# Optimization experiments

Hardware: AMD Instinct MI355X
Metric: run time of the kernel (lower is better)

Reference implementation:

```python
import jax, jax.numpy as jnp
import numpy as np

MODEL_DIM = 1024
TOTAL_DIM = 1024
N_HEADS = 16
HEAD_DIM = TOTAL_DIM // N_HEADS


def setup_inputs() -> dict:
    key = jax.random.key(0)
    k1, k2, k3 = jax.random.split(key, 3)
    query = jax.random.normal(k1, (2, 2048, MODEL_DIM), dtype=jnp.float32)
    # nn.Linear(model_dim, 3*total_dim, bias=False): store as [in, out] for x @ W
    W_in = jax.random.normal(k2, (MODEL_DIM, 3 * TOTAL_DIM), dtype=jnp.float32) / np.sqrt(MODEL_DIM)
    W_out = jax.random.normal(k3, (TOTAL_DIM, MODEL_DIM), dtype=jnp.float32) / np.sqrt(TOTAL_DIM)
    return {"query": query, "W_in": W_in, "W_out": W_out}


def reference(query, W_in, W_out):
    B, S, _ = query.shape
    qkv = query @ W_in                      # [B, S, 3*D]
    q, k, v = jnp.split(qkv, 3, axis=-1)    # each [B, S, D]

    def to_heads(t):
        return t.reshape(B, S, N_HEADS, HEAD_DIM).transpose(0, 2, 1, 3)  # [B,H,S,d]

    q, k, v = to_heads(q), to_heads(k), to_heads(v)
    scale = 1.0 / np.sqrt(HEAD_DIM).astype(np.float32)
    scores = jnp.einsum('bhqd,bhkd->bhqk', q, k) * scale  # [B,H,S,S]
    causal = jnp.tril(jnp.ones((S, S), dtype=bool))
    scores = jnp.where(causal, scores, jnp.finfo(scores.dtype).min)
    probs = jax.nn.softmax(scores, axis=-1)
    attn = jnp.einsum('bhqk,bhkd->bhqd', probs, v)        # [B,H,S,d]
    attn = attn.transpose(0, 2, 1, 3).reshape(B, S, TOTAL_DIM)
    return attn @ W_out                     # [B, S, model_dim]
```

## Files before the change

kernel.cpp:

```cpp
#include <hip/hip_runtime.h>


typedef __bf16 bf16x8 __attribute__((ext_vector_type(8)));
typedef __bf16 bf16x4 __attribute__((ext_vector_type(4)));
typedef short s16x4 __attribute__((ext_vector_type(4)));
typedef float f32x4 __attribute__((ext_vector_type(4)));
typedef int i32x2 __attribute__((ext_vector_type(2)));

#define B_   2
#define S_   2048
#define DM   1024
#define NH   16
#define HD   64
#define N3   3072
#define M_   4096

#define SCALE_LOG2E 0.180336884f

__device__ __forceinline__ unsigned short f2bf(float f) {
  unsigned int u = __float_as_uint(f);
  u += 0x7fffu + ((u >> 16) & 1u);
  return (unsigned short)(u >> 16);
}

__device__ __forceinline__ void gload_lds16(void* lds, const void* g) {
  __builtin_amdgcn_global_load_lds(
      (__attribute__((address_space(1))) void*)g,
      (__attribute__((address_space(3))) void*)lds, 16, 0, 0);
}

__device__ __forceinline__ f32x4 mfma16(bf16x4 a, bf16x4 b, f32x4 c) {
#if __has_builtin(__builtin_amdgcn_mfma_f32_16x16x16_bf16)
  return __builtin_amdgcn_mfma_f32_16x16x16_bf16(a, b, c, 0, 0, 0);
#else
  return __builtin_amdgcn_mfma_f32_16x16x16bf16_1k(
      __builtin_bit_cast(s16x4, a), __builtin_bit_cast(s16x4, b), c, 0, 0, 0);
#endif
}

__global__ __launch_bounds__(256) void f32_to_bf16_vec(
    const float4* __restrict__ in, unsigned short* __restrict__ out, int n4) {
  int i = blockIdx.x * 256 + threadIdx.x;
  if (i < n4) {
    float4 v = in[i];
    ushort4 o;
    o.x = f2bf(v.x); o.y = f2bf(v.y); o.z = f2bf(v.z); o.w = f2bf(v.w);
    *(ushort4*)(&out[(size_t)i * 4]) = o;
  }
}

__global__ __launch_bounds__(256) void transpose_f32_bf16(
    const float* __restrict__ in, unsigned short* __restrict__ out, int R, int C,
    int scale_rows, float scale) {
  __shared__ float tile[32][33];
  const int tx = threadIdx.x, ty = threadIdx.y;
  const int x = blockIdx.x * 32 + tx;
  const int y0 = blockIdx.y * 32;
#pragma unroll
  for (int j = 0; j < 32; j += 8)
    tile[ty + j][tx] = in[(size_t)(y0 + ty + j) * C + x];
  __syncthreads();
  const int ox = y0 + tx;
  const int oy0 = blockIdx.x * 32;
#pragma unroll
  for (int j = 0; j < 32; j += 8) {
    const int orow = oy0 + ty + j;
    float v = tile[tx][ty + j];
    if (orow < scale_rows) v *= scale;
    out[(size_t)orow * R + ox] = f2bf(v);
  }
}

__global__ __launch_bounds__(256) void transpose_v(
    const unsigned short* __restrict__ qkv, unsigned short* __restrict__ vTn) {
  __shared__ unsigned short tile[64][72];
  const int kt = blockIdx.x;
  const int h  = blockIdx.y;
  const int b  = blockIdx.z;
  const int t  = threadIdx.x;
  const int row = t >> 3;
  const int c8  = (t & 7) * 8;
#pragma unroll
  for (int rr = 0; rr < 2; rr++) {
    const int s = row + rr * 32;
    const size_t src = (size_t)(b * S_ + kt * 64 + s) * N3 + 2 * DM + h * HD + c8;
    *(float4*)&tile[s][c8] = *(const float4*)&qkv[src];
  }
  __syncthreads();
  const size_t base = (size_t)((b * NH + h) * 32 + kt) * 4096;
#pragma unroll
  for (int u0 = 0; u0 < 2; u0++) {
    const int u = t + u0 * 256;
    const int p = u >> 8, d = (u >> 2) & 63, q = u & 3;
    const int s0 = 32 * p + q * 4;
    ushort4 w0, w1;
    w0.x = tile[s0 + 0][d];  w0.y = tile[s0 + 1][d];
    w0.z = tile[s0 + 2][d];  w0.w = tile[s0 + 3][d];
    w1.x = tile[s0 + 16][d]; w1.y = tile[s0 + 17][d];
    w1.z = tile[s0 + 18][d]; w1.w = tile[s0 + 19][d];
    *(ushort4*)&vTn[base + (size_t)u * 8]     = w0;
    *(ushort4*)&vTn[base + (size_t)u * 8 + 4] = w1;
  }
}

template <int OUT_BF16>
__global__ __launch_bounds__(256) void gemm_abt(
    const unsigned short* __restrict__ A, const unsigned short* __restrict__ Bt,
    void* __restrict__ Cv, int M, int N, int K) {
  __shared__ __align__(16) unsigned short a_sm[128 * 32];
  __shared__ __align__(16) unsigned short b_sm[128 * 32];
  const int tid = threadIdx.x;
  const int lane = tid & 63, wave = tid >> 6;
  const int quad = lane >> 4, l15 = lane & 15;
  const int row0 = blockIdx.y * 128, col0 = blockIdx.x * 128;
  const int wm = (wave >> 1) * 64, wn = (wave & 1) * 64;

  f32x4 acc[4][4];
#pragma unroll
  for (int i = 0; i < 4; i++)
#pragma unroll
    for (int j = 0; j < 4; j++) acc[i][j] = (f32x4){0.f, 0.f, 0.f, 0.f};

  const int e0 = tid * 8;

  for (int k0 = 0; k0 < K; k0 += 32) {
    __syncthreads();
#pragma unroll
    for (int i = 0; i < 2; i++) {
      int e = e0 + i * 2048;
      int r = e >> 5, c = e & 31;
      gload_lds16(&a_sm[e], &A[(size_t)(row0 + r) * K + k0 + c]);
      gload_lds16(&b_sm[e], &Bt[(size_t)(col0 + r) * K + k0 + c]);
    }
    __syncthreads();

    bf16x8 af[4], bfb[4];
#pragma unroll
    for (int i = 0; i < 4; i++) {
      af[i]  = *(const bf16x8*)&a_sm[(wm + i * 16 + l15) * 32 + quad * 8];
      bfb[i] = *(const bf16x8*)&b_sm[(wn + i * 16 + l15) * 32 + quad * 8];
    }
#pragma unroll
    for (int i = 0; i < 4; i++)
#pragma unroll
      for (int j = 0; j < 4; j++)
        acc[i][j] = __builtin_amdgcn_mfma_f32_16x16x32_bf16(af[i], bfb[j], acc[i][j], 0, 0, 0);
  }

#pragma unroll
  for (int i = 0; i < 4; i++) {
#pragma unroll
    for (int j = 0; j < 4; j++) {
#pragma unroll
      for (int r = 0; r < 4; r++) {
        const int row = row0 + wm + i * 16 + quad * 4 + r;
        const int col = col0 + wn + j * 16 + l15;
        const float v = acc[i][j][r];
        if (OUT_BF16)
          ((unsigned short*)Cv)[(size_t)row * N + col] = f2bf(v);
        else
          ((float*)Cv)[(size_t)row * N + col] = v;
      }
    }
  }
}

__global__ __launch_bounds__(512, 4) void attn_fused11(
    const unsigned short* __restrict__ qkv,
    const unsigned short* __restrict__ vTn,
    unsigned short* __restrict__ attnout) {
  const int h = blockIdx.y, b = blockIdx.z;
  const int j = blockIdx.x;
  const int tid = threadIdx.x;
  const int lane = tid & 63, wave = tid >> 6;
  const int quad = lane >> 4, l15 = lane & 15;
  const int sw = l15 & 7;

  __shared__ __align__(16) unsigned short k_sm[4 * 4096];
  __shared__ __align__(16) unsigned short vt_sm[4 * 4096];

  const int wrow0 = (wave < 4) ? (j * 64 + wave * 16)
                               : ((31 - j) * 64 + (wave - 4) * 16);
  const int qrow = wrow0 + l15;

  bf16x8 qf[2];
  {
    const unsigned short* qp = qkv + (size_t)(b * S_ + qrow) * N3 + h * HD + quad * 8;
    qf[0] = *(const bf16x8*)qp;
    qf[1] = *(const bf16x8*)(qp + 32);
  }

  f32x4 o[4];
#pragma unroll
  for (int n = 0; n < 4; n++) o[n] = (f32x4){0.f, 0.f, 0.f, 0.f};
  float lsum = 0.f;

  const int r0s = tid >> 3;
  const int gch = ((tid & 7) ^ (r0s & 7)) * 8;
  const unsigned short* kgb = qkv + (size_t)(b * S_ + r0s) * N3 + DM + h * HD + gch;
  const unsigned short* vgl = vTn + (size_t)((b * NH + h) * 32) * 4096 + tid * 8;

  const int nt = 32 - j;

  int pk[4][2];
  const unsigned short* vbp = &vt_sm[0];

  auto PV = [&]() {
#pragma unroll
    for (int p = 0; p < 2; p++) {
      i32x2 wlo, whi;
      wlo.x = pk[2 * p][0];     wlo.y = pk[2 * p][1];
      whi.x = pk[2 * p + 1][0]; whi.y = pk[2 * p + 1][1];
      const bf16x4 blo = __builtin_bit_cast(bf16x4, wlo);
      const bf16x4 bhi = __builtin_bit_cast(bf16x4, whi);
#pragma unroll
      for (int mb = 0; mb < 4; mb++) {
        const bf16x8 vv =
            *(const bf16x8*)&vbp[(p * 256 + mb * 64 + l15 * 4 + quad) * 8];
        bf16x4 alo, ahi;
#pragma unroll
        for (int i = 0; i < 4; i++) { alo[i] = vv[i]; ahi[i] = vv[i + 4]; }
        o[mb] = mfma16(alo, blo, o[mb]);
        o[mb] = mfma16(ahi, bhi, o[mb]);
      }
    }
  };

  gload_lds16(&k_sm[tid * 8], kgb);
  gload_lds16(&vt_sm[tid * 8], vgl);
  gload_lds16(&k_sm[4096 + tid * 8], kgb + (size_t)64 * N3);
  gload_lds16(&vt_sm[4096 + tid * 8], vgl + 4096);

  for (int t = 0; t < nt; t++) {
    if (t + 1 < nt) asm volatile("s_waitcnt vmcnt(2)" ::: "memory");
    else            asm volatile("s_waitcnt vmcnt(0)" ::: "memory");
    __builtin_amdgcn_s_barrier();
    __builtin_amdgcn_sched_barrier(0);
    if (t + 2 < nt) {
      const int b2 = (t + 2) & 3;
      gload_lds16(&k_sm[b2 * 4096 + tid * 8], kgb + (size_t)(t + 2) * 64 * N3);
      gload_lds16(&vt_sm[b2 * 4096 + tid * 8], vgl + (size_t)(t + 2) * 4096);
    }
    const unsigned short* kb = &k_sm[(t & 3) * 4096];
    const unsigned short* vb = &vt_sm[(t & 3) * 4096];

    if (t >= 1 && (t - 1) * 64 <= wrow0 + 15) PV();

    if (t * 64 <= wrow0 + 15) {
      f32x4 s[4];
#pragma unroll
      for (int mb = 0; mb < 4; mb++) s[mb] = (f32x4){0.f, 0.f, 0.f, 0.f};
#pragma unroll
      for (int mb = 0; mb < 4; mb++) {
        const int ro = (mb * 16 + l15) * 64;
        bf16x8 kf0 = *(const bf16x8*)&kb[ro + ((quad ^ sw) << 3)];
        bf16x8 kf1 = *(const bf16x8*)&kb[ro + (((4 + quad) ^ sw) << 3)];
        s[mb] = __builtin_amdgcn_mfma_f32_16x16x32_bf16(kf0, qf[0], s[mb], 0, 0, 0);
        s[mb] = __builtin_amdgcn_mfma_f32_16x16x32_bf16(kf1, qf[1], s[mb], 0, 0, 0);
      }

      if (t * 64 + 63 <= wrow0) {
#pragma unroll
        for (int mb = 0; mb < 4; mb++)
#pragma unroll
          for (int r = 0; r < 4; r++)
            s[mb][r] = exp2f(s[mb][r]);
      } else {
        const int kq0 = t * 64 + quad * 4;
#pragma unroll
        for (int mb = 0; mb < 4; mb++)
#pragma unroll
          for (int r = 0; r < 4; r++) {
            const float e = exp2f(s[mb][r]);
            s[mb][r] = (kq0 + mb * 16 + r <= qrow) ? e : 0.f;
          }
      }
#pragma unroll
      for (int mb = 0; mb < 4; mb++)
        lsum += (s[mb][0] + s[mb][1]) + (s[mb][2] + s[mb][3]);

#pragma unroll
      for (int mb = 0; mb < 4; mb++) {
        const unsigned u0 = __float_as_uint(s[mb][0]) + 0x8000u;
        const unsigned u1 = __float_as_uint(s[mb][1]) + 0x8000u;
        const unsigned u2 = __float_as_uint(s[mb][2]) + 0x8000u;
        const unsigned u3 = __float_as_uint(s[mb][3]) + 0x8000u;
        pk[mb][0] = (int)__builtin_amdgcn_perm(u1, u0, 0x07060302u);
        pk[mb][1] = (int)__builtin_amdgcn_perm(u3, u2, 0x07060302u);
      }
      vbp = vb;
    }
  }

  if ((nt - 1) * 64 <= wrow0 + 15) PV();

  asm volatile("s_waitcnt vmcnt(0)" ::: "memory");

  float l = lsum;
  l += __shfl_xor(l, 16);
  l += __shfl_xor(l, 32);
  const float inv = 1.0f / l;
  const size_t grow = (size_t)(b * S_ + qrow);
#pragma unroll
  for (int mb = 0; mb < 4; mb++) {
    ushort4 w;
    w.x = f2bf(o[mb][0] * inv);
    w.y = f2bf(o[mb][1] * inv);
    w.z = f2bf(o[mb][2] * inv);
    w.w = f2bf(o[mb][3] * inv);
    *(ushort4*)&attnout[grow * DM + h * HD + mb * 16 + quad * 4] = w;
  }
}

extern "C" void kernel_launch(void* const* d_in, const int* in_sizes, int n_in,
                              void* d_out, int out_size, void* d_ws, size_t ws_size,
                              hipStream_t stream) {
  const float* query = (const float*)d_in[0];
  const float* w_in  = (const float*)d_in[1];
  const float* w_out = (const float*)d_in[2];
  float* out = (float*)d_out;

  char* ws = (char*)d_ws;
  unsigned short* qbf     = (unsigned short*)(ws);
  unsigned short* vTn     = (unsigned short*)(ws);
  unsigned short* w_in_t  = (unsigned short*)(ws + 8388608);
  unsigned short* w_out_t = (unsigned short*)(ws + 14680064);
  unsigned short* qkv     = (unsigned short*)(ws + 16777216);
  unsigned short* attn    = (unsigned short*)(ws + 41943040);

  f32_to_bf16_vec<<<dim3(M_ * DM / 1024), dim3(256), 0, stream>>>(
      (const float4*)query, qbf, M_ * DM / 4);
  transpose_f32_bf16<<<dim3(N3 / 32, DM / 32), dim3(32, 8), 0, stream>>>(
      w_in, w_in_t, DM, N3, DM, SCALE_LOG2E);
  transpose_f32_bf16<<<dim3(DM / 32, DM / 32), dim3(32, 8), 0, stream>>>(
      w_out, w_out_t, DM, DM, 0, 1.0f);
  gemm_abt<1><<<dim3(N3 / 128, M_ / 128), dim3(256), 0, stream>>>(qbf, w_in_t, qkv, M_, N3, DM);
  transpose_v<<<dim3(32, NH, B_), dim3(256), 0, stream>>>(qkv, vTn);
  attn_fused11<<<dim3(16, NH, B_), dim3(512), 0, stream>>>(qkv, vTn, attn);
  gemm_abt<0><<<dim3(DM / 128, M_ / 128), dim3(256), 0, stream>>>(attn, w_out_t, out, M_, DM, DM);
}
```

Before: 198.8 us.

## Use 64-row tiles for output GEMM, add MFMA priority and hardware bf16 pack

Replaces the output projection GEMM with a 64x128-tile variant, doubling the grid to 512 blocks so more CUs are busy on the 4096x1024 problem. In attention, the MFMA sections are wrapped with s_setprio so waves issuing matrix ops get scheduling priority. The manual add-and-permute bf16 packing is replaced with the v_cvt_pk_bf16_f32 instruction, which uses round-to-nearest-even instead of round-half-up. The new GEMM has no double buffering and synchronises twice per K step, which may cost latency hiding.

```diff
diff --git a/kernel.cpp b/kernel.cpp
--- a/kernel.cpp
+++ b/kernel.cpp
@@ -36,6 +36,12 @@
   return __builtin_amdgcn_mfma_f32_16x16x16bf16_1k(
       __builtin_bit_cast(s16x4, a), __builtin_bit_cast(s16x4, b), c, 0, 0, 0);
 #endif
+}
+
+__device__ __forceinline__ int cvtpk(float s0, float s1) {
+  int r;
+  asm("v_cvt_pk_bf16_f32 %0, %1, %2" : "=v"(r) : "v"(s0), "v"(s1));
+  return r;
 }
 
 __global__ __launch_bounds__(256) void f32_to_bf16_vec(
@@ -165,7 +171,68 @@
   }
 }
 
-__global__ __launch_bounds__(512, 4) void attn_fused11(
+__global__ __launch_bounds__(256) void gemm_abt_64(
+    const unsigned short* __restrict__ A, const unsigned short* __restrict__ Bt,
+    float* __restrict__ C, int M, int N, int K) {
+  __shared__ __align__(16) unsigned short a_sm[64 * 32];
+  __shared__ __align__(16) unsigned short b_sm[128 * 32];
+  const int tid = threadIdx.x;
+  const int lane = tid & 63, wave = tid >> 6;
+  const int quad = lane >> 4, l15 = lane & 15;
+  const int row0 = blockIdx.y * 64, col0 = blockIdx.x * 128;
+  const int wn = wave * 32;
+
+  f32x4 acc[4][2];
+#pragma unroll
+  for (int i = 0; i < 4; i++)
+#pragma unroll
+    for (int j = 0; j < 2; j++) acc[i][j] = (f32x4){0.f, 0.f, 0.f, 0.f};
+
+  const int e0 = tid * 8;
+
+  for (int k0 = 0; k0 < K; k0 += 32) {
+    __syncthreads();
+    {
+      const int r = e0 >> 5, c = e0 & 31;
+      gload_lds16(&a_sm[e0], &A[(size_t)(row0 + r) * K + k0 + c]);
+    }
+#pragma unroll
+    for (int i = 0; i < 2; i++) {
+      int e = e0 + i * 2048;
+      int r = e >> 5, c = e & 31;
+      gload_lds16(&b_sm[e], &Bt[(size_t)(col0 + r) * K + k0 + c]);
+    }
+    __syncthreads();
+
+    bf16x8 af[4], bfb[2];
+#pragma unroll
+    for (int i = 0; i < 4; i++)
+      af[i] = *(const bf16x8*)&a_sm[(i * 16 + l15) * 32 + quad * 8];
+#pragma unroll
+    for (int j = 0; j < 2; j++)
+      bfb[j] = *(const bf16x8*)&b_sm[(wn + j * 16 + l15) * 32 + quad * 8];
+#pragma unroll
+    for (int i = 0; i < 4; i++)
+#pragma unroll
+      for (int j = 0; j < 2; j++)
+        acc[i][j] = __builtin_amdgcn_mfma_f32_16x16x32_bf16(af[i], bfb[j], acc[i][j], 0, 0, 0);
+  }
+
+#pragma unroll
+  for (int i = 0; i < 4; i++) {
+#pragma unroll
+    for (int j = 0; j < 2; j++) {
+#pragma unroll
+      for (int r = 0; r < 4; r++) {
+        const int row = row0 + i * 16 + quad * 4 + r;
+        const int col = col0 + wn + j * 16 + l15;
+        C[(size_t)row * N + col] = acc[i][j][r];
+      }
+    }
+  }
+}
+
+__global__ __launch_bounds__(512, 4) void attn_fused12(
     const unsigned short* __restrict__ qkv,
     const unsigned short* __restrict__ vTn,
     unsigned short* __restrict__ attnout) {
@@ -206,6 +273,7 @@
   const unsigned short* vbp = &vt_sm[0];
 
   auto PV = [&]() {
+    __builtin_amdgcn_s_setprio(1);
 #pragma unroll
     for (int p = 0; p < 2; p++) {
       i32x2 wlo, whi;
@@ -224,6 +292,7 @@
         o[mb] = mfma16(ahi, bhi, o[mb]);
       }
     }
+    __builtin_amdgcn_s_setprio(0);
   };
 
   gload_lds16(&k_sm[tid * 8], kgb);
@@ -250,6 +319,7 @@
       f32x4 s[4];
 #pragma unroll
       for (int mb = 0; mb < 4; mb++) s[mb] = (f32x4){0.f, 0.f, 0.f, 0.f};
+      __builtin_amdgcn_s_setprio(1);
 #pragma unroll
       for (int mb = 0; mb < 4; mb++) {
         const int ro = (mb * 16 + l15) * 64;
@@ -258,6 +328,7 @@
         s[mb] = __builtin_amdgcn_mfma_f32_16x16x32_bf16(kf0, qf[0], s[mb], 0, 0, 0);
         s[mb] = __builtin_amdgcn_mfma_f32_16x16x32_bf16(kf1, qf[1], s[mb], 0, 0, 0);
       }
+      __builtin_amdgcn_s_setprio(0);
 
       if (t * 64 + 63 <= wrow0) {
 #pragma unroll
@@ -281,12 +352,8 @@
 
 #pragma unroll
       for (int mb = 0; mb < 4; mb++) {
-        const unsigned u0 = __float_as_uint(s[mb][0]) + 0x8000u;
-        const unsigned u1 = __float_as_uint(s[mb][1]) + 0x8000u;
-        const unsigned u2 = __float_as_uint(s[mb][2]) + 0x8000u;
-        const unsigned u3 = __float_as_uint(s[mb][3]) + 0x8000u;
-        pk[mb][0] = (int)__builtin_amdgcn_perm(u1, u0, 0x07060302u);
-        pk[mb][1] = (int)__builtin_amdgcn_perm(u3, u2, 0x07060302u);
+        pk[mb][0] = cvtpk(s[mb][0], s[mb][1]);
+        pk[mb][1] = cvtpk(s[mb][2], s[mb][3]);
       }
       vbp = vb;
     }
@@ -336,6 +403,6 @@
       w_out, w_out_t, DM, DM, 0, 1.0f);
   gemm_abt<1><<<dim3(N3 / 128, M_ / 128), dim3(256), 0, stream>>>(qbf, w_in_t, qkv, M_, N3, DM);
   transpose_v<<<dim3(32, NH, B_), dim3(256), 0, stream>>>(qkv, vTn);
-  attn_fused11<<<dim3(16, NH, B_), dim3(512), 0, stream>>>(qkv, vTn, attn);
-  gemm_abt<0><<<dim3(DM / 128, M_ / 128), dim3(256), 0, stream>>>(attn, w_out_t, out, M_, DM, DM);
-}
+  attn_fused12<<<dim3(16, NH, B_), dim3(512), 0, stream>>>(qkv, vTn, attn);
+  gemm_abt_64<<<dim3(DM / 128, M_ / 64), dim3(256), 0, stream>>>(attn, w_out_t, out, M_, DM, DM);
+}
```

Result: faster. 194.6 us (-2.1%).
